# Kernel tuning notes

Hardware: AMD Instinct MI355X
Metric: run time of the kernel (lower is better)

The kernel has to match this reference:

```python
import jax, jax.numpy as jnp
import numpy as np

NUM_GROUPS = 8
EPS = 1e-5


def setup_inputs() -> dict:
    key = jax.random.key(0)
    ks = jax.random.split(key, 3)
    B, C, H, W = 32, 256, 64, 64
    x = jax.random.normal(ks[0], (B, C, H, W), dtype=jnp.float32)
    gn_weight = jnp.ones((C,), dtype=jnp.float32)
    gn_bias = jnp.zeros((C,), dtype=jnp.float32)
    # 1x1 convs stored as [out_ch, in_ch] matrices (kernel dims squeezed)
    qkv_weight = jax.random.normal(ks[1], (3 * C, C), dtype=jnp.float32) * (1.0 / np.sqrt(C))
    qkv_bias = jnp.zeros((3 * C,), dtype=jnp.float32)
    proj_weight = jax.random.normal(ks[2], (C, C), dtype=jnp.float32) * (1.0 / np.sqrt(C))
    proj_bias = jnp.zeros((C,), dtype=jnp.float32)
    return {
        "x": x,
        "gn_weight": gn_weight,
        "gn_bias": gn_bias,
        "qkv_weight": qkv_weight,
        "qkv_bias": qkv_bias,
        "proj_weight": proj_weight,
        "proj_bias": proj_bias,
    }


def _group_norm(x, weight, bias):
    B, C, H, W = x.shape
    g = x.reshape(B, NUM_GROUPS, C // NUM_GROUPS, H, W)
    mean = g.mean(axis=(2, 3, 4), keepdims=True)
    var = g.var(axis=(2, 3, 4), keepdims=True)
    g = (g - mean) * jax.lax.rsqrt(var + EPS)
    x = g.reshape(B, C, H, W)
    return x * weight[None, :, None, None] + bias[None, :, None, None]


def reference(x, gn_weight, gn_bias, qkv_weight, qkv_bias, proj_weight, proj_bias):
    B, C, H, W = x.shape
    x_norm = _group_norm(x, gn_weight, gn_bias)
    # 1x1 conv C -> 3C: contraction over channel dim
    qkv = jnp.einsum('bchw,oc->bohw', x_norm, qkv_weight) + qkv_bias[None, :, None, None]
    qkv = qkv.reshape(B, 3, C, H * W)  # [B,3,C,HW]
    q, k, v = qkv[:, 0], qkv[:, 1], qkv[:, 2]  # each [B,C,HW]
    # channel attention: attn is [B,C,C], softmax over last (key-channel) dim
    scale = 1.0 / jnp.sqrt(jnp.asarray(C, dtype=x.dtype))
    scores = jnp.einsum('bcn,bdn->bcd', q, k) * scale
    attn = jax.nn.softmax(scores, axis=-1)
    out = jnp.einsum('bcd,bdn->bcn', attn, v).reshape(B, C, H, W)
    proj = jnp.einsum('bchw,oc->bohw', out, proj_weight) + proj_bias[None, :, None, None]
    return x + proj
```

## Files before the change

kernel.cpp:

```cpp
#include <hip/hip_runtime.h>


#define B_ 32
#define C_ 256
#define N_ 4096
#define GSIZE (32 * N_)
#define EPSV 1e-5f
#define SCALE 0.0625f

#define OFF_SC    0
#define OFF_SH    8192
#define OFF_RS    16384
#define OFF_RSP   24576
#define OFF_SQP   90112
#define OFF_RALL  155648
#define OFF_UV    180224
#define OFF_CV    212992
#define OFF_CONST 221184
#define OFF_WVT   229376
#define OFF_GH    262144
#define OFF_GL    1310720
#define OFF_AT    2359296
#define OFF_S16   4456448
#define OFF_GP    5505024

typedef _Float16 half_t;
typedef half_t f16x8 __attribute__((ext_vector_type(8)));
typedef float f32x16 __attribute__((ext_vector_type(16)));

#define GBAR()                                             \
  do {                                                     \
    asm volatile("s_waitcnt lgkmcnt(0)" ::: "memory");     \
    __builtin_amdgcn_sched_barrier(0);                     \
    __builtin_amdgcn_s_barrier();                          \
  } while (0)

__global__ __launch_bounds__(1024, 4) void gram_v7_k(
    const float* __restrict__ x, float* __restrict__ ws) {
  __shared__ __align__(16) char hb[2][32768];
  int b = blockIdx.x >> 3, ks = blockIdx.x & 7;
  int t = threadIdx.x;
  const float* xb = x + (size_t)b * (C_ * (size_t)N_) + ks * 512;
  int lane = t & 63, w = t >> 6;
  int wm = w >> 2, wn = w & 3, r31 = lane & 31, hi = lane >> 5;
  int lrow = t >> 4, lc4 = t & 15;
  const float* lbase = xb + (size_t)lrow * N_ + lc4 * 4;
  f32x16 acc[2][2] = {};
  float4 stg[2][4];
  float rs[4] = {0.f, 0.f, 0.f, 0.f};
  float rq[4] = {0.f, 0.f, 0.f, 0.f};

#define LOADV(sb, c)                                                      \
  _Pragma("unroll") for (int p = 0; p < 4; ++p)                           \
      stg[sb][p] = *(const float4*)(lbase + (size_t)p * 64 * N_ + (c) * 64);

#define WRITEV(sb, buf)                                                   \
  {                                                                       \
    char* bp = hb[buf];                                                   \
    _Pragma("unroll") for (int p = 0; p < 4; ++p) {                       \
      float4 v = stg[sb][p];                                              \
      rs[p] += v.x + v.y + v.z + v.w;                                     \
      rq[p] += v.x * v.x + v.y * v.y + v.z * v.z + v.w * v.w;             \
      union { half_t h[4]; uint2 u; } H;                                  \
      H.h[0] = (half_t)v.x; H.h[1] = (half_t)v.y;                         \
      H.h[2] = (half_t)v.z; H.h[3] = (half_t)v.w;                         \
      int row = lrow + p * 64;                                            \
      int slot = (lc4 >> 1) ^ (row & 7);                                  \
      *(uint2*)(bp + row * 128 + slot * 16 + (lc4 & 1) * 8) = H.u;        \
    }                                                                     \
  }

  LOADV(0, 0);
  LOADV(1, 1);
  WRITEV(0, 0);
  GBAR();
  for (int c = 0; c < 8; ++c) {
    int buf = c & 1;
    __builtin_amdgcn_s_setprio(1);
#pragma unroll
    for (int kk = 0; kk < 4; ++kk) {
      int kb = kk * 32 + hi * 16;
      f16x8 Af[2], Bf[2];
#pragma unroll
      for (int m = 0; m < 2; ++m) {
        int row = wm * 64 + m * 32 + r31;
        Af[m] = *(const f16x8*)(hb[buf] + row * 128 + (((kb >> 4) ^ (row & 7)) * 16));
      }
#pragma unroll
      for (int n = 0; n < 2; ++n) {
        int row = wn * 64 + n * 32 + r31;
        Bf[n] = *(const f16x8*)(hb[buf] + row * 128 + (((kb >> 4) ^ (row & 7)) * 16));
      }
#pragma unroll
      for (int m = 0; m < 2; ++m)
#pragma unroll
        for (int n = 0; n < 2; ++n)
          acc[m][n] = __builtin_amdgcn_mfma_f32_32x32x16_f16(Af[m], Bf[n], acc[m][n], 0, 0, 0);
    }
    __builtin_amdgcn_s_setprio(0);
    if (c < 7) {
      int nb = (c + 1) & 1;
      WRITEV(nb, nb);
      if (c < 6) LOADV(buf, c + 2);
      GBAR();
    }
  }
#pragma unroll
  for (int p = 0; p < 4; ++p) {
    float s = rs[p], q = rq[p];
    s += __shfl_xor(s, 1); s += __shfl_xor(s, 2);
    s += __shfl_xor(s, 4); s += __shfl_xor(s, 8);
    q += __shfl_xor(q, 1); q += __shfl_xor(q, 2);
    q += __shfl_xor(q, 4); q += __shfl_xor(q, 8);
    if ((t & 15) == 0) {
      int row = lrow + p * 64;
      ws[OFF_RSP + (size_t)blockIdx.x * 256 + row] = s;
      ws[OFF_SQP + (size_t)blockIdx.x * 256 + row] = q;
    }
  }
  half_t* Gp = (half_t*)(ws + OFF_GP) + (size_t)blockIdx.x * 65536;
#pragma unroll
  for (int m = 0; m < 2; ++m)
#pragma unroll
    for (int n = 0; n < 2; ++n)
#pragma unroll
      for (int r = 0; r < 16; ++r) {
        int gr = wm * 64 + m * 32 + (r & 3) + 8 * (r >> 2) + 4 * hi;
        int gc = wn * 64 + n * 32 + r31;
        Gp[gr * 256 + gc] = (half_t)acc[m][n][r];
      }
#undef LOADV
#undef WRITEV
}

__global__ __launch_bounds__(256) void gsum2_k(float* __restrict__ ws) {
  int bx = blockIdx.x;
  int b = bx >> 6, seg = bx & 63;
  int e0 = seg * 1024 + threadIdx.x * 4;
  const half_t* Gp = (const half_t*)(ws + OFF_GP) + (size_t)b * 8 * 65536 + e0;
  float s[4] = {0.f, 0.f, 0.f, 0.f};
#pragma unroll
  for (int ks = 0; ks < 8; ++ks) {
    union { uint2 u; half_t h[4]; } P;
    P.u = *(const uint2*)(Gp + (size_t)ks * 65536);
#pragma unroll
    for (int i = 0; i < 4; ++i) s[i] += (float)P.h[i];
  }
  union { half_t h[4]; uint2 u; } H, L;
#pragma unroll
  for (int i = 0; i < 4; ++i) {
    H.h[i] = (half_t)s[i];
    L.h[i] = (half_t)(s[i] - (float)H.h[i]);
  }
  *(uint2*)((half_t*)(ws + OFF_GH) + (size_t)b * 65536 + e0) = H.u;
  *(uint2*)((half_t*)(ws + OFF_GL) + (size_t)b * 65536 + e0) = L.u;
}

__global__ __launch_bounds__(256) void prep2_k(const float* __restrict__ gw,
                                               const float* __restrict__ gb,
                                               const float* __restrict__ qkvw,
                                               float* __restrict__ ws) {
  int b = blockIdx.x, t = threadIdx.x;
  __shared__ float sL[256], qL[256], svecs[256], scrs[256], shsm[256];
  __shared__ float gmean[8], grstd[8];
  float s = 0.f, q = 0.f;
#pragma unroll
  for (int ks = 0; ks < 8; ++ks) {
    s += ws[OFF_RSP + (b * 8 + ks) * 256 + t];
    q += ws[OFF_SQP + (b * 8 + ks) * 256 + t];
  }
  ws[OFF_RS + b * 256 + t] = s;
  sL[t] = s; qL[t] = q;
  __syncthreads();
  if (t < 8) {
    float gs = 0.f, gq = 0.f;
    for (int i = 0; i < 32; ++i) { gs += sL[t * 32 + i]; gq += qL[t * 32 + i]; }
    float mean = gs * (1.f / GSIZE);
    float var = gq * (1.f / GSIZE) - mean * mean;
    gmean[t] = mean;
    grstd[t] = rsqrtf(var + EPSV);
  }
  __syncthreads();
  int g = t >> 5;
  float sc = grstd[g] * gw[t];
  float sh = gb[t] - gmean[g] * sc;
  ws[OFF_SC + b * 256 + t] = sc;
  ws[OFF_SH + b * 256 + t] = sh;
  svecs[t] = s * sc + 4096.f * sh;
  scrs[t] = s * sc;
  shsm[t] = sh;
  __syncthreads();
  {
    const float* r1 = qkvw + (size_t)t * 256;
    float rq = 0.f, uq = 0.f, vq = 0.f;
#pragma unroll 4
    for (int c = 0; c < 256; ++c) {
      float wv = r1[c];
      rq += wv * svecs[c]; uq += wv * scrs[c]; vq += wv * shsm[c];
    }
    ws[OFF_RALL + b * 768 + t] = rq;
    ws[OFF_UV + b * 1024 + t] = uq;
    ws[OFF_UV + b * 1024 + 256 + t] = vq;
  }
  {
    const float* r2 = qkvw + (size_t)(256 + t) * 256;
    float rk = 0.f, uk = 0.f, vk = 0.f;
#pragma unroll 4
    for (int c = 0; c < 256; ++c) {
      float wv = r2[c];
      rk += wv * svecs[c]; uk += wv * scrs[c]; vk += wv * shsm[c];
    }
    ws[OFF_RALL + b * 768 + 256 + t] = rk;
    ws[OFF_UV + b * 1024 + 512 + t] = uk;
    ws[OFF_UV + b * 1024 + 768 + t] = vk;
  }
}

__global__ __launch_bounds__(256) void wvt2_k(const float* __restrict__ qkvw,
                                              float* __restrict__ ws) {
  __shared__ float sm[64][68];
  int be = blockIdx.x * 64, bd = blockIdx.y * 64;
  int t = threadIdx.x;
#pragma unroll
  for (int i = 0; i < 4; ++i) {
    int f = t + i * 256;
    int row = f >> 4, c4 = f & 15;
    float4 v = *(const float4*)(qkvw + (size_t)(512 + bd + row) * 256 + be + c4 * 4);
    sm[row][c4 * 4 + 0] = v.x; sm[row][c4 * 4 + 1] = v.y;
    sm[row][c4 * 4 + 2] = v.z; sm[row][c4 * 4 + 3] = v.w;
  }
  __syncthreads();
  half_t* WVT = (half_t*)(ws + OFF_WVT);
#pragma unroll
  for (int i = 0; i < 4; ++i) {
    int f = t + i * 256;
    int el = f >> 4, d4 = (f & 15) * 4;
    union { half_t h[4]; uint2 u; } P;
#pragma unroll
    for (int k = 0; k < 4; ++k) P.h[k] = (half_t)sm[d4 + k][el];
    *(uint2*)(WVT + (size_t)(be + el) * 256 + bd + d4) = P.u;
  }
}

__global__ __launch_bounds__(256) void logits2_k(
    const float* __restrict__ qkvw, const float* __restrict__ qkvb,
    float* __restrict__ ws) {
  int b = blockIdx.y, r0 = blockIdx.x * 32;
  int t = threadIdx.x, lane = t & 63, w = t >> 6, r31 = lane & 31, hi = lane >> 5;
  __shared__ __align__(16) char GHL[32768];
  __shared__ __align__(16) char AHL[8192];
  __shared__ float T1s[32][257];
  __shared__ float scs[256];
  __shared__ float bk_s[256], rk_s[256], uk_s[256], vk_s[256];
  __shared__ float bq_s[32], rq_s[32], uq_s[32], vq_s[32];
  scs[t] = ws[OFF_SC + b * 256 + t];
  bk_s[t] = qkvb[256 + t];
  rk_s[t] = ws[OFF_RALL + b * 768 + 256 + t];
  uk_s[t] = ws[OFF_UV + b * 1024 + 512 + t];
  vk_s[t] = ws[OFF_UV + b * 1024 + 768 + t];
  if (t < 32) {
    bq_s[t] = qkvb[r0 + t];
    rq_s[t] = ws[OFF_RALL + b * 768 + r0 + t];
    uq_s[t] = ws[OFF_UV + b * 1024 + r0 + t];
    vq_s[t] = ws[OFF_UV + b * 1024 + 256 + r0 + t];
  }
  __syncthreads();
  const half_t* Gh = (const half_t*)(ws + OFF_GH) + (size_t)b * 65536;
  const half_t* Gl = (const half_t*)(ws + OFF_GL) + (size_t)b * 65536;
  f32x16 acc[2] = {};
  for (int k0 = 0; k0 < 256; k0 += 32) {
    {
      int row = t >> 3, c4 = t & 7;
      float4 v = *(const float4*)(qkvw + (size_t)(r0 + row) * 256 + k0 + c4 * 4);
      union { half_t h[4]; uint2 u; } H;
      H.h[0] = (half_t)(v.x * scs[k0 + c4 * 4 + 0]);
      H.h[1] = (half_t)(v.y * scs[k0 + c4 * 4 + 1]);
      H.h[2] = (half_t)(v.z * scs[k0 + c4 * 4 + 2]);
      H.h[3] = (half_t)(v.w * scs[k0 + c4 * 4 + 3]);
      int s8 = row & 7;
      *(uint2*)(AHL + row * 128 + (((c4 >> 1) ^ s8) * 16) + (c4 & 1) * 8) = H.u;
    }
    {
#pragma unroll
      for (int p = 0; p < 8; ++p) {
        int f = t + p * 256;
        int row = f >> 3, ko = f & 7;
        const half_t* src = (ko < 4) ? Gh : Gl;
        uint4 v = *(const uint4*)(src + (size_t)row * 256 + k0 + (ko & 3) * 8);
        *(uint4*)(GHL + row * 128 + ((ko ^ (row & 7)) * 16)) = v;
      }
    }
    __syncthreads();
#pragma unroll
    for (int kk = 0; kk < 2; ++kk) {
      int kb = kk * 32 + hi * 16;
      int arow = r31;
      f16x8 Aq = *(const f16x8*)(AHL + arow * 128 + (((kb >> 4) ^ (arow & 7)) * 16));
#pragma unroll
      for (int n = 0; n < 2; ++n) {
        int row = w * 64 + n * 32 + r31;
        int s8 = row & 7;
        f16x8 Bh = *(const f16x8*)(GHL + row * 128 + (((kb >> 4) ^ s8) * 16));
        f16x8 Bl = *(const f16x8*)(GHL + row * 128 + ((((kb >> 4) + 4) ^ s8) * 16));
        acc[n] = __builtin_amdgcn_mfma_f32_32x32x16_f16(Aq, Bh, acc[n], 0, 0, 0);
        acc[n] = __builtin_amdgcn_mfma_f32_32x32x16_f16(Aq, Bl, acc[n], 0, 0, 0);
      }
    }
    __syncthreads();
  }
#pragma unroll
  for (int n = 0; n < 2; ++n)
#pragma unroll
    for (int r = 0; r < 16; ++r)
      T1s[(r & 3) + 8 * (r >> 2) + 4 * hi][w * 64 + n * 32 + r31] = acc[n][r];
  __syncthreads();
  f32x16 acc2[2] = {};
  for (int k0 = 0; k0 < 256; k0 += 64) {
    {
      int row = t >> 3;
#pragma unroll
      for (int u = 0; u < 2; ++u) {
        int c4 = (t & 7) + u * 8;
        float vv[4];
#pragma unroll
        for (int j = 0; j < 4; ++j) vv[j] = T1s[row][k0 + c4 * 4 + j];
        union { half_t h[4]; uint2 u2; } H, L;
#pragma unroll
        for (int j = 0; j < 4; ++j) {
          half_t h = (half_t)vv[j];
          H.h[j] = h; L.h[j] = (half_t)(vv[j] - (float)h);
        }
        int s16 = row & 15;
        *(uint2*)(AHL + row * 256 + (((c4 >> 1) ^ s16) * 16) + (c4 & 1) * 8) = H.u2;
        *(uint2*)(AHL + row * 256 + ((((c4 >> 1) + 8) ^ s16) * 16) + (c4 & 1) * 8) = L.u2;
      }
    }
    {
#pragma unroll
      for (int p = 0; p < 16; ++p) {
        int f = t + p * 256;
        int row = f >> 4, c4 = f & 15;
        float4 v = *(const float4*)(qkvw + (size_t)(256 + row) * 256 + k0 + c4 * 4);
        union { half_t h[4]; uint2 u; } H;
        H.h[0] = (half_t)(v.x * scs[k0 + c4 * 4 + 0]);
        H.h[1] = (half_t)(v.y * scs[k0 + c4 * 4 + 1]);
        H.h[2] = (half_t)(v.z * scs[k0 + c4 * 4 + 2]);
        H.h[3] = (half_t)(v.w * scs[k0 + c4 * 4 + 3]);
        int slot = (c4 >> 1) ^ (row & 7);
        *(uint2*)(GHL + row * 128 + slot * 16 + (c4 & 1) * 8) = H.u;
      }
    }
    __syncthreads();
#pragma unroll
    for (int kk = 0; kk < 4; ++kk) {
      int kb = kk * 32 + hi * 16;
      int arow = r31;
      int s16 = arow & 15;
      f16x8 Ah = *(const f16x8*)(AHL + arow * 256 + (((kb >> 4) ^ s16) * 16));
      f16x8 Al = *(const f16x8*)(AHL + arow * 256 + ((((kb >> 4) + 8) ^ s16) * 16));
#pragma unroll
      for (int n = 0; n < 2; ++n) {
        int row = w * 64 + n * 32 + r31;
        f16x8 Bf = *(const f16x8*)(GHL + row * 128 + (((kb >> 4) ^ (row & 7)) * 16));
        acc2[n] = __builtin_amdgcn_mfma_f32_32x32x16_f16(Ah, Bf, acc2[n], 0, 0, 0);
        acc2[n] = __builtin_amdgcn_mfma_f32_32x32x16_f16(Al, Bf, acc2[n], 0, 0, 0);
      }
    }
    __syncthreads();
  }
#pragma unroll
  for (int n = 0; n < 2; ++n)
#pragma unroll
    for (int r = 0; r < 16; ++r) {
      int rr = (r & 3) + 8 * (r >> 2) + 4 * hi;
      int cc = w * 64 + n * 32 + r31;
      float v = acc2[n][r];
      float ukv = uk_s[cc] + 4096.f * vk_s[cc];
      v = (v + uq_s[rr] * vk_s[cc] + vq_s[rr] * ukv + bq_s[rr] * rk_s[cc] +
           bk_s[cc] * (rq_s[rr] + 4096.f * bq_s[rr])) * SCALE;
      T1s[rr][cc] = v;
    }
  __syncthreads();
  bk_s[t] = qkvb[512 + t];
  __syncthreads();
  {
    int row = t >> 3, ls = t & 7;
    float m = -1e30f;
#pragma unroll
    for (int i = 0; i < 32; ++i) m = fmaxf(m, T1s[row][ls + i * 8]);
    m = fmaxf(m, __shfl_xor(m, 1));
    m = fmaxf(m, __shfl_xor(m, 2));
    m = fmaxf(m, __shfl_xor(m, 4));
    float s = 0.f, cvp = 0.f;
#pragma unroll
    for (int i = 0; i < 32; ++i) {
      int col = ls + i * 8;
      float e = __expf(T1s[row][col] - m);
      T1s[row][col] = e;
      s += e;
      cvp += e * bk_s[col];
    }
    s += __shfl_xor(s, 1); s += __shfl_xor(s, 2); s += __shfl_xor(s, 4);
    cvp += __shfl_xor(cvp, 1); cvp += __shfl_xor(cvp, 2); cvp += __shfl_xor(cvp, 4);
    float inv = 1.f / s;
#pragma unroll
    for (int i = 0; i < 32; ++i) T1s[row][ls + i * 8] *= inv;
    if (ls == 0) ws[OFF_CV + b * 256 + r0 + row] = cvp * inv;
  }
  __syncthreads();
  {
    float* ATb = ws + OFF_AT + (size_t)b * 65536;
#pragma unroll
    for (int u = 0; u < 8; ++u) {
      float4 v = {T1s[u * 4 + 0][t], T1s[u * 4 + 1][t], T1s[u * 4 + 2][t],
                  T1s[u * 4 + 3][t]};
      *(float4*)(ATb + (size_t)t * 256 + r0 + u * 4) = v;
    }
  }
}

__global__ __launch_bounds__(256) void fused_s_k(const float* __restrict__ pw,
                                                 const float* __restrict__ pb,
                                                 float* __restrict__ ws) {
  int b = blockIdx.y, r0 = blockIdx.x * 32;
  int t = threadIdx.x, lane = t & 63, w = t >> 6, r31 = lane & 31, hi = lane >> 5;
  __shared__ __align__(16) char GHL[32768];
  __shared__ __align__(16) char AHL[8192];
  __shared__ float T1s[32][257];
  __shared__ float cvs[256], scv[256], shv[256];
  cvs[t] = ws[OFF_CV + b * 256 + t];
  scv[t] = ws[OFF_SC + b * 256 + t];
  shv[t] = ws[OFF_SH + b * 256 + t];
  __syncthreads();
  const float* ATb = ws + OFF_AT + (size_t)b * 65536;
  f32x16 acc[2] = {};
  for (int k0 = 0; k0 < 256; k0 += 64) {
    {
#pragma unroll
      for (int p = 0; p < 2; ++p) {
        int f = t + p * 256;
        int row = f >> 4, c4 = f & 15;
        float4 v = *(const float4*)(pw + (size_t)(r0 + row) * 256 + k0 + c4 * 4);
        union { half_t h[4]; uint2 u; } H;
        H.h[0] = (half_t)v.x; H.h[1] = (half_t)v.y;
        H.h[2] = (half_t)v.z; H.h[3] = (half_t)v.w;
        int slot = (c4 >> 1) ^ (row & 7);
        *(uint2*)(AHL + row * 128 + slot * 16 + (c4 & 1) * 8) = H.u;
      }
    }
    {
#pragma unroll
      for (int p = 0; p < 16; ++p) {
        int f = t + p * 256;
        int row = f >> 4, c4 = f & 15;
        float4 v = *(const float4*)(ATb + (size_t)row * 256 + k0 + c4 * 4);
        union { half_t h[4]; uint2 u; } H;
        H.h[0] = (half_t)v.x; H.h[1] = (half_t)v.y;
        H.h[2] = (half_t)v.z; H.h[3] = (half_t)v.w;
        int slot = (c4 >> 1) ^ (row & 7);
        *(uint2*)(GHL + row * 128 + slot * 16 + (c4 & 1) * 8) = H.u;
      }
    }
    __syncthreads();
#pragma unroll
    for (int kk = 0; kk < 4; ++kk) {
      int kb = kk * 32 + hi * 16;
      int arow = r31;
      f16x8 Af = *(const f16x8*)(AHL + arow * 128 + (((kb >> 4) ^ (arow & 7)) * 16));
#pragma unroll
      for (int n = 0; n < 2; ++n) {
        int row = w * 64 + n * 32 + r31;
        f16x8 Bf = *(const f16x8*)(GHL + row * 128 + (((kb >> 4) ^ (row & 7)) * 16));
        acc[n] = __builtin_amdgcn_mfma_f32_32x32x16_f16(Af, Bf, acc[n], 0, 0, 0);
      }
    }
    __syncthreads();
  }
#pragma unroll
  for (int n = 0; n < 2; ++n)
#pragma unroll
    for (int r = 0; r < 16; ++r)
      T1s[(r & 3) + 8 * (r >> 2) + 4 * hi][w * 64 + n * 32 + r31] = acc[n][r];
  __syncthreads();
  float cfull = 0.f;
  {
    int row = t >> 3, ls = t & 7;
    float a = 0.f;
#pragma unroll
    for (int i = 0; i < 32; ++i) {
      int c = ls + i * 8;
      a += pw[(size_t)(r0 + row) * 256 + c] * cvs[c];
    }
    a += __shfl_xor(a, 1); a += __shfl_xor(a, 2); a += __shfl_xor(a, 4);
    cfull = a + pb[r0 + row];
  }
  const half_t* WVT = (const half_t*)(ws + OFF_WVT);
  f32x16 acc2[2] = {};
  for (int k0 = 0; k0 < 256; k0 += 64) {
    {
      int row = t >> 3;
#pragma unroll
      for (int u = 0; u < 2; ++u) {
        int c4 = (t & 7) + u * 8;
        float vv[4];
#pragma unroll
        for (int j = 0; j < 4; ++j) vv[j] = T1s[row][k0 + c4 * 4 + j];
        union { half_t h[4]; uint2 u2; } H, L;
#pragma unroll
        for (int j = 0; j < 4; ++j) {
          half_t h = (half_t)vv[j];
          H.h[j] = h; L.h[j] = (half_t)(vv[j] - (float)h);
        }
        int s16 = row & 15;
        *(uint2*)(AHL + row * 256 + (((c4 >> 1) ^ s16) * 16) + (c4 & 1) * 8) = H.u2;
        *(uint2*)(AHL + row * 256 + ((((c4 >> 1) + 8) ^ s16) * 16) + (c4 & 1) * 8) = L.u2;
      }
    }
    {
#pragma unroll
      for (int p = 0; p < 8; ++p) {
        int f = t + p * 256;
        int row = f >> 3, h8 = f & 7;
        uint2 v = *(const uint2*)(WVT + (size_t)row * 256 + k0 + h8 * 8);
        uint2 v2 = *(const uint2*)(WVT + (size_t)row * 256 + k0 + h8 * 8 + 4);
        int slot = h8 ^ (row & 7);
        *(uint2*)(GHL + row * 128 + slot * 16) = v;
        *(uint2*)(GHL + row * 128 + slot * 16 + 8) = v2;
      }
    }
    __syncthreads();
#pragma unroll
    for (int kk = 0; kk < 4; ++kk) {
      int kb = kk * 32 + hi * 16;
      int arow = r31;
      int s16 = arow & 15;
      f16x8 Ah = *(const f16x8*)(AHL + arow * 256 + (((kb >> 4) ^ s16) * 16));
      f16x8 Al = *(const f16x8*)(AHL + arow * 256 + ((((kb >> 4) + 8) ^ s16) * 16));
#pragma unroll
      for (int n = 0; n < 2; ++n) {
        int row = w * 64 + n * 32 + r31;
        f16x8 Bf = *(const f16x8*)(GHL + row * 128 + (((kb >> 4) ^ (row & 7)) * 16));
        acc2[n] = __builtin_amdgcn_mfma_f32_32x32x16_f16(Ah, Bf, acc2[n], 0, 0, 0);
        acc2[n] = __builtin_amdgcn_mfma_f32_32x32x16_f16(Al, Bf, acc2[n], 0, 0, 0);
      }
    }
    __syncthreads();
  }
#pragma unroll
  for (int n = 0; n < 2; ++n)
#pragma unroll
    for (int r = 0; r < 16; ++r)
      T1s[(r & 3) + 8 * (r >> 2) + 4 * hi][w * 64 + n * 32 + r31] = acc2[n][r];
  __syncthreads();
  {
    half_t* Sb = (half_t*)(ws + OFF_S16) + (size_t)b * 65536;
    int row = t >> 3, seg = t & 7;
    float dsh = 0.f;
#pragma unroll
    for (int u = 0; u < 4; ++u) {
      union { half_t h[8]; uint4 v; } P;
#pragma unroll
      for (int j = 0; j < 8; ++j) {
        int col = seg * 32 + u * 8 + j;
        float sv = T1s[row][col];
        dsh += sv * shv[col];
        P.h[j] = (half_t)(sv * scv[col]);
      }
      *(uint4*)(Sb + (size_t)(r0 + row) * 256 + seg * 32 + u * 8) = P.v;
    }
    dsh += __shfl_xor(dsh, 1); dsh += __shfl_xor(dsh, 2); dsh += __shfl_xor(dsh, 4);
    if (seg == 0) ws[OFF_CONST + b * 256 + r0 + row] = cfull + dsh;
  }
}

__global__ __launch_bounds__(256, 4) void final_v4_k(
    const float* __restrict__ x, float* __restrict__ out,
    const float* __restrict__ ws) {
  __shared__ __align__(16) char xs[32768];
  int b = blockIdx.y, n0 = blockIdx.x * 64;
  int t = threadIdx.x, lane = t & 63, w = t >> 6;
  int r31 = lane & 31, hi = lane >> 5;
  const half_t* Sb = (const half_t*)(ws + OFF_S16) + (size_t)b * 65536;
  const float* xb = x + (size_t)b * (C_ * (size_t)N_);
  {
    int n4 = (t & 15) * 4, cb = (t >> 4) * 4;
#pragma unroll
    for (int p = 0; p < 4; ++p) {
      int c = cb + p * 64;
      float a[4][4];
#pragma unroll
      for (int i = 0; i < 4; ++i) {
        float4 v = *(const float4*)(xb + (size_t)(c + i) * N_ + n0 + n4);
        a[i][0] = v.x; a[i][1] = v.y; a[i][2] = v.z; a[i][3] = v.w;
      }
#pragma unroll
      for (int j = 0; j < 4; ++j) {
        int n = n4 + j;
        union { half_t h[4]; uint2 u; } P;
        P.h[0] = (half_t)a[0][j]; P.h[1] = (half_t)a[1][j];
        P.h[2] = (half_t)a[2][j]; P.h[3] = (half_t)a[3][j];
        int g = ((cb >> 3) & 7) ^ ((n >> 3) & 7) ^ (n & 7);
        *(uint2*)(xs + p * 8192 + n * 128 + g * 16 + (cb & 7) * 2) = P.u;
      }
    }
  }
  __syncthreads();
  f32x16 acc[2][2] = {};
  int obase = w * 64;
  const half_t* Arow0 = Sb + (size_t)(obase + r31) * 256;
  const half_t* Arow1 = Sb + (size_t)(obase + 32 + r31) * 256;
  f16x8 An0[2], An1[2];
  An0[0] = *(const f16x8*)(Arow0 + hi * 8);
  An0[1] = *(const f16x8*)(Arow1 + hi * 8);
  An1[0] = *(const f16x8*)(Arow0 + 16 + hi * 8);
  An1[1] = *(const f16x8*)(Arow1 + 16 + hi * 8);
#pragma unroll
  for (int kk = 0; kk < 16; ++kk) {
    f16x8 Af[2];
    if (kk & 1) { Af[0] = An1[0]; Af[1] = An1[1]; }
    else        { Af[0] = An0[0]; Af[1] = An0[1]; }
    if (kk < 14) {
      int ck2 = (kk + 2) * 16 + hi * 8;
      if (kk & 1) { An1[0] = *(const f16x8*)(Arow0 + ck2); An1[1] = *(const f16x8*)(Arow1 + ck2); }
      else        { An0[0] = *(const f16x8*)(Arow0 + ck2); An0[1] = *(const f16x8*)(Arow1 + ck2); }
    }
    int ck = kk * 16 + hi * 8;
    int q = ck >> 6, ch = (ck >> 3) & 7;
    f16x8 Bf[2];
#pragma unroll
    for (int n = 0; n < 2; ++n) {
      int col = n * 32 + r31;
      int g = ch ^ ((col >> 3) & 7) ^ (col & 7);
      Bf[n] = *(const f16x8*)(xs + q * 8192 + col * 128 + g * 16);
    }
#pragma unroll
    for (int m = 0; m < 2; ++m)
#pragma unroll
      for (int n = 0; n < 2; ++n)
        acc[m][n] = __builtin_amdgcn_mfma_f32_32x32x16_f16(Af[m], Bf[n], acc[m][n], 0, 0, 0);
  }
  float* ob = out + (size_t)b * (C_ * (size_t)N_);
  const float* cstb = ws + OFF_CONST + b * 256;
#pragma unroll
  for (int m = 0; m < 2; ++m)
#pragma unroll
    for (int r = 0; r < 16; ++r) {
      int o = obase + m * 32 + (r & 3) + 8 * (r >> 2) + 4 * hi;
      float cv = cstb[o];
      size_t base = (size_t)o * N_ + n0;
      int q = o >> 6, ch = (o >> 3) & 7;
#pragma unroll
      for (int n = 0; n < 2; ++n) {
        int col = n * 32 + r31;
        int g = ch ^ ((col >> 3) & 7) ^ (col & 7);
        float xr = (float)*(const half_t*)(xs + q * 8192 + col * 128 + g * 16 + (o & 7) * 2);
        ob[base + col] = acc[m][n][r] + xr + cv;
      }
    }
}

extern "C" void kernel_launch(void* const* d_in, const int* in_sizes, int n_in,
                              void* d_out, int out_size, void* d_ws,
                              size_t ws_size, hipStream_t stream) {
  const float* x = (const float*)d_in[0];
  const float* gw = (const float*)d_in[1];
  const float* gb = (const float*)d_in[2];
  const float* qkvw = (const float*)d_in[3];
  const float* qkvb = (const float*)d_in[4];
  const float* pw = (const float*)d_in[5];
  const float* pb = (const float*)d_in[6];
  float* out = (float*)d_out;
  float* ws = (float*)d_ws;

  hipLaunchKernelGGL(gram_v7_k, dim3(256), dim3(1024), 0, stream, x, ws);
  hipLaunchKernelGGL(prep2_k, dim3(32), dim3(256), 0, stream, gw, gb, qkvw, ws);
  hipLaunchKernelGGL(gsum2_k, dim3(2048), dim3(256), 0, stream, ws);
  hipLaunchKernelGGL(wvt2_k, dim3(4, 4), dim3(256), 0, stream, qkvw, ws);
  hipLaunchKernelGGL(logits2_k, dim3(8, 32), dim3(256), 0, stream, qkvw, qkvb, ws);
  hipLaunchKernelGGL(fused_s_k, dim3(8, 32), dim3(256), 0, stream, pw, pb, ws);
  hipLaunchKernelGGL(final_v4_k, dim3(64, 32), dim3(256), 0, stream, x, out, ws);
}
```

Before: 211.1 us.

## Stage gram K-chunks in two large LDS passes instead of double-buffered pipeline

The gram kernel now loads 256 columns per pass into a 128 KB LDS tile, in two passes, instead of streaming eight 64-column chunks through a register-staged double buffer. Each thread loads 64 contiguous floats per row with a wider 32-way XOR swizzle, and the row-sum reductions shrink to a 4-lane shuffle. The aim is fewer barriers and larger, more contiguous loads per thread. In exchange, load/compute overlap within a block is lost and the 128 KB LDS footprint limits each CU to a single block of 1024 threads.

New measurement: 270.4 us. +28.1%, slower.

```diff
diff --git a/kernel.cpp b/kernel.cpp
--- a/kernel.cpp
+++ b/kernel.cpp
@@ -28,68 +28,51 @@
 typedef half_t f16x8 __attribute__((ext_vector_type(8)));
 typedef float f32x16 __attribute__((ext_vector_type(16)));
 
-#define GBAR()                                             \
-  do {                                                     \
-    asm volatile("s_waitcnt lgkmcnt(0)" ::: "memory");     \
-    __builtin_amdgcn_sched_barrier(0);                     \
-    __builtin_amdgcn_s_barrier();                          \
-  } while (0)
-
-__global__ __launch_bounds__(1024, 4) void gram_v7_k(
+__global__ __launch_bounds__(1024, 4) void gram_v8_k(
     const float* __restrict__ x, float* __restrict__ ws) {
-  __shared__ __align__(16) char hb[2][32768];
+  __shared__ __align__(16) char xs[131072];
   int b = blockIdx.x >> 3, ks = blockIdx.x & 7;
   int t = threadIdx.x;
   const float* xb = x + (size_t)b * (C_ * (size_t)N_) + ks * 512;
   int lane = t & 63, w = t >> 6;
   int wm = w >> 2, wn = w & 3, r31 = lane & 31, hi = lane >> 5;
-  int lrow = t >> 4, lc4 = t & 15;
-  const float* lbase = xb + (size_t)lrow * N_ + lc4 * 4;
+  int srow = t >> 2, scc = t & 3;
+  const float* sbase = xb + (size_t)srow * N_ + scc * 64;
   f32x16 acc[2][2] = {};
-  float4 stg[2][4];
-  float rs[4] = {0.f, 0.f, 0.f, 0.f};
-  float rq[4] = {0.f, 0.f, 0.f, 0.f};
-
-#define LOADV(sb, c)                                                      \
-  _Pragma("unroll") for (int p = 0; p < 4; ++p)                           \
-      stg[sb][p] = *(const float4*)(lbase + (size_t)p * 64 * N_ + (c) * 64);
-
-#define WRITEV(sb, buf)                                                   \
-  {                                                                       \
-    char* bp = hb[buf];                                                   \
-    _Pragma("unroll") for (int p = 0; p < 4; ++p) {                       \
-      float4 v = stg[sb][p];                                              \
-      rs[p] += v.x + v.y + v.z + v.w;                                     \
-      rq[p] += v.x * v.x + v.y * v.y + v.z * v.z + v.w * v.w;             \
-      union { half_t h[4]; uint2 u; } H;                                  \
-      H.h[0] = (half_t)v.x; H.h[1] = (half_t)v.y;                         \
-      H.h[2] = (half_t)v.z; H.h[3] = (half_t)v.w;                         \
-      int row = lrow + p * 64;                                            \
-      int slot = (lc4 >> 1) ^ (row & 7);                                  \
-      *(uint2*)(bp + row * 128 + slot * 16 + (lc4 & 1) * 8) = H.u;        \
-    }                                                                     \
-  }
-
-  LOADV(0, 0);
-  LOADV(1, 1);
-  WRITEV(0, 0);
-  GBAR();
-  for (int c = 0; c < 8; ++c) {
-    int buf = c & 1;
+  float rs = 0.f, rq = 0.f;
+  int swz = srow * 512 + (scc & 3) * 0;
+  for (int pass = 0; pass < 2; ++pass) {
+    const float* pbase = sbase + pass * 256;
+#pragma unroll
+    for (int ii = 0; ii < 8; ++ii) {
+      float4 v0 = *(const float4*)(pbase + ii * 8);
+      float4 v1 = *(const float4*)(pbase + ii * 8 + 4);
+      rs += v0.x + v0.y + v0.z + v0.w + v1.x + v1.y + v1.z + v1.w;
+      rq += v0.x * v0.x + v0.y * v0.y + v0.z * v0.z + v0.w * v0.w +
+            v1.x * v1.x + v1.y * v1.y + v1.z * v1.z + v1.w * v1.w;
+      union { half_t h[8]; uint4 u; } P;
+      P.h[0] = (half_t)v0.x; P.h[1] = (half_t)v0.y;
+      P.h[2] = (half_t)v0.z; P.h[3] = (half_t)v0.w;
+      P.h[4] = (half_t)v1.x; P.h[5] = (half_t)v1.y;
+      P.h[6] = (half_t)v1.z; P.h[7] = (half_t)v1.w;
+      int gcol = scc * 8 + ii;
+      *(uint4*)(xs + srow * 512 + ((gcol ^ (srow & 31)) << 4)) = P.u;
+    }
+    __syncthreads();
     __builtin_amdgcn_s_setprio(1);
 #pragma unroll
-    for (int kk = 0; kk < 4; ++kk) {
-      int kb = kk * 32 + hi * 16;
+    for (int kk = 0; kk < 16; ++kk) {
+      int gk = kk * 2 + hi;
       f16x8 Af[2], Bf[2];
 #pragma unroll
       for (int m = 0; m < 2; ++m) {
         int row = wm * 64 + m * 32 + r31;
-        Af[m] = *(const f16x8*)(hb[buf] + row * 128 + (((kb >> 4) ^ (row & 7)) * 16));
+        Af[m] = *(const f16x8*)(xs + row * 512 + ((gk ^ (row & 31)) << 4));
       }
 #pragma unroll
       for (int n = 0; n < 2; ++n) {
         int row = wn * 64 + n * 32 + r31;
-        Bf[n] = *(const f16x8*)(hb[buf] + row * 128 + (((kb >> 4) ^ (row & 7)) * 16));
+        Bf[n] = *(const f16x8*)(xs + row * 512 + ((gk ^ (row & 31)) << 4));
       }
 #pragma unroll
       for (int m = 0; m < 2; ++m)
@@ -98,25 +81,13 @@
           acc[m][n] = __builtin_amdgcn_mfma_f32_32x32x16_f16(Af[m], Bf[n], acc[m][n], 0, 0, 0);
     }
     __builtin_amdgcn_s_setprio(0);
-    if (c < 7) {
-      int nb = (c + 1) & 1;
-      WRITEV(nb, nb);
-      if (c < 6) LOADV(buf, c + 2);
-      GBAR();
-    }
-  }
-#pragma unroll
-  for (int p = 0; p < 4; ++p) {
-    float s = rs[p], q = rq[p];
-    s += __shfl_xor(s, 1); s += __shfl_xor(s, 2);
-    s += __shfl_xor(s, 4); s += __shfl_xor(s, 8);
-    q += __shfl_xor(q, 1); q += __shfl_xor(q, 2);
-    q += __shfl_xor(q, 4); q += __shfl_xor(q, 8);
-    if ((t & 15) == 0) {
-      int row = lrow + p * 64;
-      ws[OFF_RSP + (size_t)blockIdx.x * 256 + row] = s;
-      ws[OFF_SQP + (size_t)blockIdx.x * 256 + row] = q;
-    }
+    if (pass == 0) __syncthreads();
+  }
+  rs += __shfl_xor(rs, 1); rs += __shfl_xor(rs, 2);
+  rq += __shfl_xor(rq, 1); rq += __shfl_xor(rq, 2);
+  if ((t & 3) == 0) {
+    ws[OFF_RSP + (size_t)blockIdx.x * 256 + srow] = rs;
+    ws[OFF_SQP + (size_t)blockIdx.x * 256 + srow] = rq;
   }
   half_t* Gp = (half_t*)(ws + OFF_GP) + (size_t)blockIdx.x * 65536;
 #pragma unroll
@@ -129,8 +100,6 @@
         int gc = wn * 64 + n * 32 + r31;
         Gp[gr * 256 + gc] = (half_t)acc[m][n][r];
       }
-#undef LOADV
-#undef WRITEV
 }
 
 __global__ __launch_bounds__(256) void gsum2_k(float* __restrict__ ws) {
@@ -672,7 +641,7 @@
   float* out = (float*)d_out;
   float* ws = (float*)d_ws;
 
-  hipLaunchKernelGGL(gram_v7_k, dim3(256), dim3(1024), 0, stream, x, ws);
+  hipLaunchKernelGGL(gram_v8_k, dim3(256), dim3(1024), 0, stream, x, ws);
   hipLaunchKernelGGL(prep2_k, dim3(32), dim3(256), 0, stream, gw, gb, qkvw, ws);
   hipLaunchKernelGGL(gsum2_k, dim3(2048), dim3(256), 0, stream, ws);
   hipLaunchKernelGGL(wvt2_k, dim3(4, 4), dim3(256), 0, stream, qkvw, ws);
```
